# Optimization experiments

Measured on AMD Instinct MI355X. Metric: run time of the kernel, lower is better.

The kernel has to match this reference:

```python
import jax, jax.numpy as jnp
import numpy as np

NUM_HEADS = 8
DIM = 256
NW = 64  # number of windows per batch element


def setup_inputs() -> dict:
    key = jax.random.key(0)
    k_x, k_m, k_ws, k_wm, k_wp, k_bp = jax.random.split(key, 6)
    B_, N, C = 512, 128, DIM
    x = jax.random.normal(k_x, (B_, N, C), dtype=jnp.float32)
    # 0 / -100 additive attention mask (stand-in for the 0/-inf shift-window mask)
    mask = jnp.where(jax.random.uniform(k_m, (NW, N, N)) < 0.5, 0.0, -100.0).astype(jnp.float32)
    std = 0.02
    w_qkv_self = jax.random.normal(k_ws, (3 * C, C), dtype=jnp.float32) * std
    w_qkv_mut = jax.random.normal(k_wm, (3 * C, C), dtype=jnp.float32) * std
    w_proj = jax.random.normal(k_wp, (C, 2 * C), dtype=jnp.float32) * std
    b_proj = jax.random.normal(k_bp, (C,), dtype=jnp.float32) * std
    return {"x": x, "mask": mask, "w_qkv_self": w_qkv_self,
            "w_qkv_mut": w_qkv_mut, "w_proj": w_proj, "b_proj": b_proj}


def _split_qkv(x, w):
    # x: (B_, N, C); w: (3C, C) torch Linear weight -> y = x @ w.T
    B_, N, C = x.shape
    d = C // NUM_HEADS
    qkv = (x @ w.T).reshape(B_, N, 3, NUM_HEADS, d).transpose(2, 0, 3, 1, 4)
    return qkv[0], qkv[1], qkv[2]  # each (B_, H, N, d)


def _attention(q, k, v, mask, scale):
    # q,k,v: (B_, H, n, d); mask: (nW, Nfull, Nfull) additive
    B_, H, n, d = q.shape
    nW = mask.shape[0]
    attn = jnp.einsum('bhnd,bhmd->bhnm', q * scale, k)  # (B_, H, n, n)
    attn = attn.reshape(B_ // nW, nW, H, n, n) + mask[None, :, None, :n, :n]
    attn = jax.nn.softmax(attn.reshape(B_, H, n, n), axis=-1)
    out = jnp.einsum('bhnm,bhmd->bhnd', attn, v)
    return out.transpose(0, 2, 1, 3).reshape(B_, n, H * d)  # (B_, n, C)


def reference(x, mask, w_qkv_self, w_qkv_mut, w_proj, b_proj):
    B_, N, C = x.shape
    scale = (C // NUM_HEADS) ** (-0.5)
    # self window attention
    q, k, v = _split_qkv(x, w_qkv_self)
    x_out = _attention(q, k, v, mask, scale)  # (B_, N, C)
    # mutual (cross-frame) attention between the two halves of the window
    qm, km, vm = _split_qkv(x, w_qkv_mut)
    h = N // 2
    q1, q2 = qm[:, :, :h], qm[:, :, h:]
    k1, k2 = km[:, :, :h], km[:, :, h:]
    v1, v2 = vm[:, :, :h], vm[:, :, h:]
    x1_aligned = _attention(q2, k1, v1, mask, scale)  # (B_, N//2, C)
    x2_aligned = _attention(q1, k2, v2, mask, scale)  # (B_, N//2, C)
    x_mut = jnp.concatenate([x1_aligned, x2_aligned], axis=1)  # (B_, N, C)
    x_cat = jnp.concatenate([x_mut, x_out], axis=2)  # (B_, N, 2C)
    return x_cat @ w_proj.T + b_proj  # (B_, N, C)
```

## Files before the change

kernel.cpp:

```cpp
#include <hip/hip_runtime.h>
#include <stdint.h>

typedef __bf16 bf16x4 __attribute__((ext_vector_type(4)));
typedef __bf16 bf16x8 __attribute__((ext_vector_type(8)));
typedef float f32x4 __attribute__((ext_vector_type(4)));

#define DEVI __device__ __forceinline__

DEVI ushort bfbits(float f) {
  union { __bf16 b; ushort u; } v;
  v.b = (__bf16)f;
  return v.u;
}

DEVI void gload16(const void* g, void* l) {
  auto* gp = reinterpret_cast<const __attribute__((address_space(1))) uint32_t*>(
      reinterpret_cast<uintptr_t>(g));
  auto* lp = reinterpret_cast<__attribute__((address_space(3))) uint32_t*>(
      reinterpret_cast<uintptr_t>(l));
  __builtin_amdgcn_global_load_lds(gp, lp, 16, 0, 0);
}

__global__ __launch_bounds__(256) void cvt_x(const float* __restrict__ in,
                                             ushort* __restrict__ out) {
  int i = (blockIdx.x * 256 + threadIdx.x) * 4;
  float4 v = *(const float4*)(in + i);
  ushort4 o;
  o.x = bfbits(v.x); o.y = bfbits(v.y); o.z = bfbits(v.z); o.w = bfbits(v.w);
  *(ushort4*)(out + i) = o;
}

__global__ __launch_bounds__(256) void cvt_w(const float* __restrict__ ws,
                                             const float* __restrict__ wm,
                                             const float* __restrict__ wp,
                                             ushort* __restrict__ wqkv,
                                             ushort* __restrict__ wproj) {
  int i = blockIdx.x * 256 + threadIdx.x;
  if (i < 196608)       wqkv[i] = bfbits(ws[i]);
  else if (i < 393216)  wqkv[i] = bfbits(wm[i - 196608]);
  else                  wproj[i - 393216] = bfbits(wp[i - 393216]);
}

template <int KF, int NH>
DEVI void attn_body(const ushort* Qs, const ushort* Ks, const ushort* Vt,
                    ushort* Ps, const float* mrow, ushort* ob,
                    int qrow0, int kvbase, int orow0, int mrow0,
                    int lr, int lc) {
  f32x4 sacc[2][KF];
#pragma unroll
  for (int mf = 0; mf < 2; ++mf)
#pragma unroll
    for (int nf = 0; nf < KF; ++nf) sacc[mf][nf] = (f32x4){0.f, 0.f, 0.f, 0.f};

  bf16x8 aq[2];
#pragma unroll
  for (int mf = 0; mf < 2; ++mf) {
    int r = qrow0 + mf * 16 + lr;
    aq[mf] = *(const bf16x8*)(Qs + r * 32 + ((lc ^ ((r >> 1) & 3)) * 8));
  }
  __builtin_amdgcn_s_setprio(1);
#pragma unroll
  for (int nf = 0; nf < KF; ++nf) {
    int r = kvbase + nf * 16 + lr;
    bf16x8 bk = *(const bf16x8*)(Ks + r * 32 + ((lc ^ ((r >> 1) & 3)) * 8));
#pragma unroll
    for (int mf = 0; mf < 2; ++mf)
      sacc[mf][nf] = __builtin_amdgcn_mfma_f32_16x16x32_bf16(aq[mf], bk, sacc[mf][nf], 0, 0, 0);
  }
  __builtin_amdgcn_s_setprio(0);

#pragma unroll
  for (int mf = 0; mf < 2; ++mf)
#pragma unroll
    for (int nf = 0; nf < KF; ++nf)
#pragma unroll
      for (int r = 0; r < 4; ++r) {
        int row = mrow0 + mf * 16 + lc * 4 + r;
        int col = nf * 16 + lr;
        sacc[mf][nf][r] += mrow[row * 128 + col];
      }
#pragma unroll
  for (int mf = 0; mf < 2; ++mf)
#pragma unroll
    for (int r = 0; r < 4; ++r) {
      float mx = -1e30f;
#pragma unroll
      for (int nf = 0; nf < KF; ++nf) mx = fmaxf(mx, sacc[mf][nf][r]);
#pragma unroll
      for (int d = 1; d < 16; d <<= 1) mx = fmaxf(mx, __shfl_xor(mx, d));
      float s = 0.f;
#pragma unroll
      for (int nf = 0; nf < KF; ++nf) {
        float e = __expf(sacc[mf][nf][r] - mx);
        sacc[mf][nf][r] = e;
        s += e;
      }
#pragma unroll
      for (int d = 1; d < 16; d <<= 1) s += __shfl_xor(s, d);
      float inv = 1.f / s;
#pragma unroll
      for (int nf = 0; nf < KF; ++nf) sacc[mf][nf][r] *= inv;
    }

  f32x4 oacc[2][2];
#pragma unroll
  for (int mf = 0; mf < 2; ++mf)
#pragma unroll
    for (int nf = 0; nf < 2; ++nf) oacc[mf][nf] = (f32x4){0.f, 0.f, 0.f, 0.f};

#pragma unroll
  for (int hf = 0; hf < NH; ++hf) {
    __syncthreads();
#pragma unroll
    for (int mf = 0; mf < 2; ++mf)
#pragma unroll
      for (int r = 0; r < 4; ++r) {
        int prow = orow0 + mf * 16 + lc * 4 + r;
#pragma unroll
        for (int nf2 = 0; nf2 < 4; ++nf2) {
          int col = nf2 * 16 + lr;
          int grp = (col >> 3) ^ (prow & 7);
          Ps[prow * 64 + grp * 8 + (col & 7)] = bfbits(sacc[mf][hf * 4 + nf2][r]);
        }
      }
    __syncthreads();
    __builtin_amdgcn_s_setprio(1);
#pragma unroll
    for (int ks = 0; ks < 2; ++ks) {
      bf16x8 pf[2], vf[2];
#pragma unroll
      for (int mf = 0; mf < 2; ++mf) {
        int prow = orow0 + mf * 16 + lr;
        int grp = (ks * 4 + lc) ^ (prow & 7);
        pf[mf] = *(const bf16x8*)(Ps + prow * 64 + grp * 8);
      }
#pragma unroll
      for (int nf = 0; nf < 2; ++nf)
        vf[nf] = *(const bf16x8*)(Vt + (nf * 16 + lr) * 136 + kvbase + hf * 64 + ks * 32 + lc * 8);
#pragma unroll
      for (int mf = 0; mf < 2; ++mf)
#pragma unroll
        for (int nf = 0; nf < 2; ++nf)
          oacc[mf][nf] = __builtin_amdgcn_mfma_f32_16x16x32_bf16(pf[mf], vf[nf], oacc[mf][nf], 0, 0, 0);
    }
    __builtin_amdgcn_s_setprio(0);
  }

#pragma unroll
  for (int mf = 0; mf < 2; ++mf)
#pragma unroll
    for (int nf = 0; nf < 2; ++nf)
#pragma unroll
      for (int r = 0; r < 4; ++r) {
        int row = orow0 + mf * 16 + lc * 4 + r;
        int col = nf * 16 + lr;
        ob[(size_t)row * 512 + col] = bfbits(oacc[mf][nf][r]);
      }
}

__global__ __launch_bounds__(256) void attn_fused(const ushort* __restrict__ xb,
                                                  const ushort* __restrict__ wqkv,
                                                  const float* __restrict__ mask,
                                                  ushort* __restrict__ xcat) {
  __shared__ __align__(16) uint8_t smem[39424];
  ushort* Qs = (ushort*)smem;
  ushort* Vt = (ushort*)(smem + 8192);
  uint8_t* REGION = smem + 16896;
  ushort* Ks = (ushort*)REGION;
  ushort* xs = (ushort*)(REGION + 8192);
  ushort* wl = (ushort*)(REGION + 16384);
  ushort* Ps = (ushort*)REGION;

  const int bid = blockIdx.x;
  const int c = bid & 7;
  const int u = bid >> 3;
  const int m = u & 1;
  const int h = (u >> 1) & 7;
  const int b = (u >> 4) * 8 + c;
  const int wmask = b & 63;
  const int t = threadIdx.x;
  const int wid = t >> 6, l = t & 63;
  const int lr = l & 15, lc = l >> 4;
  const float scale = 0.17677669529663687f;

  const ushort* xrow = xb + (size_t)b * 128 * 256;
  const int wbase = m * 768;

  f32x4 pacc[2][6];
#pragma unroll
  for (int mf = 0; mf < 2; ++mf)
#pragma unroll
    for (int n = 0; n < 6; ++n) pacc[mf][n] = (f32x4){0.f, 0.f, 0.f, 0.f};

  for (int kk = 0; kk < 256; kk += 32) {
    __syncthreads();
#pragma unroll
    for (int p = 0; p < 2; ++p) {
      int slot = t + p * 256;
      int row = slot >> 2, cs = slot & 3;
      int cd = cs ^ ((row >> 1) & 3);
      gload16(xrow + (size_t)row * 256 + kk + cd * 8, xs + slot * 8);
    }
    {
      int slot = t;
      int row = slot >> 2, cs = slot & 3;
      int cd = cs ^ ((row >> 1) & 3);
      int grow = wbase + (row >> 5) * 256 + h * 32 + (row & 31);
      gload16(wqkv + (size_t)grow * 256 + kk + cd * 8, wl + slot * 8);
    }
    if (t < 128) {
      int slot = t + 256;
      int row = slot >> 2, cs = slot & 3;
      int cd = cs ^ ((row >> 1) & 3);
      int grow = wbase + (row >> 5) * 256 + h * 32 + (row & 31);
      gload16(wqkv + (size_t)grow * 256 + kk + cd * 8, wl + slot * 8);
    }
    __syncthreads();

    bf16x8 ax[2];
#pragma unroll
    for (int mf = 0; mf < 2; ++mf) {
      int r = wid * 32 + mf * 16 + lr;
      ax[mf] = *(const bf16x8*)(xs + r * 32 + ((lc ^ ((r >> 1) & 3)) * 8));
    }
    __builtin_amdgcn_s_setprio(1);
#pragma unroll
    for (int n = 0; n < 6; ++n) {
      int r = n * 16 + lr;
      bf16x8 bw = *(const bf16x8*)(wl + r * 32 + ((lc ^ ((r >> 1) & 3)) * 8));
#pragma unroll
      for (int mf = 0; mf < 2; ++mf)
        pacc[mf][n] = __builtin_amdgcn_mfma_f32_16x16x32_bf16(ax[mf], bw, pacc[mf][n], 0, 0, 0);
    }
    __builtin_amdgcn_s_setprio(0);
  }

#pragma unroll
  for (int mf = 0; mf < 2; ++mf) {
#pragma unroll
    for (int n = 0; n < 4; ++n)
#pragma unroll
      for (int j = 0; j < 4; ++j) {
        int row = wid * 32 + mf * 16 + lc * 4 + j;
        int d = (n & 1) * 16 + lr;
        float v = pacc[mf][n][j];
        if (n < 2) v *= scale;
        int sw = ((d >> 3) ^ ((row >> 1) & 3)) * 8 + (d & 7);
        (n < 2 ? Qs : Ks)[row * 32 + sw] = bfbits(v);
      }
#pragma unroll
    for (int k = 0; k < 2; ++k) {
      bf16x4 pk;
#pragma unroll
      for (int j = 0; j < 4; ++j) pk[j] = (__bf16)pacc[mf][4 + k][j];
      int d = k * 16 + lr;
      int row0 = wid * 32 + mf * 16 + lc * 4;
      *(bf16x4*)(Vt + d * 136 + row0) = pk;
    }
  }
  __syncthreads();

  const float* mrow = mask + (size_t)wmask * 128 * 128;

  if (m == 0) {
    ushort* ob = xcat + (size_t)b * 128 * 512 + 256 + h * 32;
    attn_body<8, 2>(Qs, Ks, Vt, Ps, mrow, ob,
                    wid * 32, 0,
                    wid * 32, wid * 32, lr, lc);
  } else {
    const int half = wid >> 1, sub = wid & 1;
    ushort* ob = xcat + (size_t)b * 128 * 512 + h * 32;
    attn_body<4, 1>(Qs, Ks, Vt, Ps, mrow, ob,
                    (half ? 0 : 64) + sub * 32, half ? 64 : 0,
                    half * 64 + sub * 32, sub * 32, lr, lc);
  }
}

__global__ __launch_bounds__(256) void gemm_proj(const ushort* __restrict__ A,
                                                 const ushort* __restrict__ B,
                                                 const float* __restrict__ bias,
                                                 float* __restrict__ out) {
  __shared__ ushort As[128 * 32];
  __shared__ ushort Bs[256 * 32];
  const int t = threadIdx.x, tm = blockIdx.x;
  const int w = t >> 6, l = t & 63;
  const int wr = (w >> 1) * 64, wc = (w & 1) * 128;
  const int lr = l & 15, lc = l >> 4;
  const ushort* Ab = A + (size_t)tm * 128 * 512;

  f32x4 acc[4][8];
#pragma unroll
  for (int m = 0; m < 4; ++m)
#pragma unroll
    for (int n = 0; n < 8; ++n) acc[m][n] = (f32x4){0.f, 0.f, 0.f, 0.f};

  for (int kk = 0; kk < 512; kk += 32) {
    __syncthreads();
#pragma unroll
    for (int p = 0; p < 2; ++p) {
      int slot = t + p * 256;
      int row = slot >> 2, cs = slot & 3;
      int cd = cs ^ ((row >> 1) & 3);
      gload16(Ab + (size_t)row * 512 + kk + cd * 8, As + slot * 8);
    }
#pragma unroll
    for (int p = 0; p < 4; ++p) {
      int slot = t + p * 256;
      int row = slot >> 2, cs = slot & 3;
      int cd = cs ^ ((row >> 1) & 3);
      gload16(B + (size_t)row * 512 + kk + cd * 8, Bs + slot * 8);
    }
    __syncthreads();

    bf16x8 af[4], bfr[8];
#pragma unroll
    for (int m = 0; m < 4; ++m) {
      int r = wr + m * 16 + lr;
      af[m] = *(const bf16x8*)(As + r * 32 + ((lc ^ ((r >> 1) & 3)) * 8));
    }
#pragma unroll
    for (int n = 0; n < 8; ++n) {
      int r = wc + n * 16 + lr;
      bfr[n] = *(const bf16x8*)(Bs + r * 32 + ((lc ^ ((r >> 1) & 3)) * 8));
    }
#pragma unroll
    for (int m = 0; m < 4; ++m)
#pragma unroll
      for (int n = 0; n < 8; ++n)
        acc[m][n] = __builtin_amdgcn_mfma_f32_16x16x32_bf16(af[m], bfr[n], acc[m][n], 0, 0, 0);
  }

#pragma unroll
  for (int m = 0; m < 4; ++m)
#pragma unroll
    for (int n = 0; n < 8; ++n)
#pragma unroll
      for (int r = 0; r < 4; ++r) {
        int row = tm * 128 + wr + m * 16 + lc * 4 + r;
        int col = wc + n * 16 + lr;
        out[(size_t)row * 256 + col] = acc[m][n][r] + bias[col];
      }
}

extern "C" void kernel_launch(void* const* d_in, const int* in_sizes, int n_in,
                              void* d_out, int out_size, void* d_ws, size_t ws_size,
                              hipStream_t stream) {
  const float* x = (const float*)d_in[0];
  const float* mask = (const float*)d_in[1];
  const float* w_qkv_self = (const float*)d_in[2];
  const float* w_qkv_mut = (const float*)d_in[3];
  const float* w_proj = (const float*)d_in[4];
  const float* b_proj = (const float*)d_in[5];
  float* out = (float*)d_out;

  uint8_t* ws = (uint8_t*)d_ws;
  ushort* xb    = (ushort*)(ws);
  ushort* wqkv  = (ushort*)(ws + 33554432);
  ushort* wproj = (ushort*)(ws + 34340864);
  ushort* xcat  = (ushort*)d_out;

  cvt_x<<<dim3(16384), dim3(256), 0, stream>>>(x, xb);
  cvt_w<<<dim3(2048), dim3(256), 0, stream>>>(w_qkv_self, w_qkv_mut, w_proj, wqkv, wproj);
  attn_fused<<<dim3(8192), dim3(256), 0, stream>>>(xb, wqkv, mask, xcat);
  gemm_proj<<<dim3(512), dim3(256), 0, stream>>>(xcat, wproj, b_proj, out);
}
```

Before: 204.2 us.

## Pre-transpose mask with log2e fold, use exp2, defer softmax normalization, prefetch QKV stage

Adds a kernel that transposes the mask per window and pre-multiplies it by log2(e), so attention can read four mask values per lane with one vector load instead of scalar strided loads. The Q scale also absorbs log2(e), which lets the softmax use the native exp2 and a reciprocal applied once to the output rather than to every probability. The QKV projection loop is restructured so the next K-slice is staged right after the MFMAs. Costs are one extra small launch and workspace buffer. The staging change only moves the load issue point, since one LDS buffer and a barrier remain between stages.

```diff
diff --git a/kernel.cpp b/kernel.cpp
--- a/kernel.cpp
+++ b/kernel.cpp
@@ -41,9 +41,33 @@
   else                  wproj[i - 393216] = bfbits(wp[i - 393216]);
 }
 
+__global__ __launch_bounds__(256) void cvt_mask(const float* __restrict__ mask,
+                                                float* __restrict__ maskT) {
+  __shared__ float tile[32][33];
+  const int w = blockIdx.x, tr = blockIdx.y, tc = blockIdx.z;
+  const float* src = mask + (size_t)w * 16384;
+  float* dst = maskT + (size_t)w * 16384;
+  const int t = threadIdx.x;
+  {
+    int r = t >> 3, c4 = (t & 7) * 4;
+    float4 v = *(const float4*)(src + (size_t)(tr * 32 + r) * 128 + tc * 32 + c4);
+    tile[r][c4 + 0] = v.x; tile[r][c4 + 1] = v.y;
+    tile[r][c4 + 2] = v.z; tile[r][c4 + 3] = v.w;
+  }
+  __syncthreads();
+  {
+    const float L2E = 1.4426950408889634f;
+    int c = t >> 3, r4 = (t & 7) * 4;
+    float4 o;
+    o.x = tile[r4 + 0][c] * L2E; o.y = tile[r4 + 1][c] * L2E;
+    o.z = tile[r4 + 2][c] * L2E; o.w = tile[r4 + 3][c] * L2E;
+    *(float4*)(dst + (size_t)(tc * 32 + c) * 128 + tr * 32 + r4) = o;
+  }
+}
+
 template <int KF, int NH>
 DEVI void attn_body(const ushort* Qs, const ushort* Ks, const ushort* Vt,
-                    ushort* Ps, const float* mrow, ushort* ob,
+                    ushort* Ps, const float* mT, ushort* ob,
                     int qrow0, int kvbase, int orow0, int mrow0,
                     int lr, int lc) {
   f32x4 sacc[2][KF];
@@ -72,13 +96,14 @@
 #pragma unroll
   for (int mf = 0; mf < 2; ++mf)
 #pragma unroll
-    for (int nf = 0; nf < KF; ++nf)
-#pragma unroll
-      for (int r = 0; r < 4; ++r) {
-        int row = mrow0 + mf * 16 + lc * 4 + r;
-        int col = nf * 16 + lr;
-        sacc[mf][nf][r] += mrow[row * 128 + col];
-      }
+    for (int nf = 0; nf < KF; ++nf) {
+      int col = nf * 16 + lr;
+      f32x4 mv = *(const f32x4*)(mT + (size_t)col * 128 + mrow0 + mf * 16 + lc * 4);
+#pragma unroll
+      for (int r = 0; r < 4; ++r) sacc[mf][nf][r] += mv[r];
+    }
+
+  float sinv[2][4];
 #pragma unroll
   for (int mf = 0; mf < 2; ++mf)
 #pragma unroll
@@ -91,15 +116,13 @@
       float s = 0.f;
 #pragma unroll
       for (int nf = 0; nf < KF; ++nf) {
-        float e = __expf(sacc[mf][nf][r] - mx);
+        float e = __builtin_amdgcn_exp2f(sacc[mf][nf][r] - mx);
         sacc[mf][nf][r] = e;
         s += e;
       }
 #pragma unroll
       for (int d = 1; d < 16; d <<= 1) s += __shfl_xor(s, d);
-      float inv = 1.f / s;
-#pragma unroll
-      for (int nf = 0; nf < KF; ++nf) sacc[mf][nf][r] *= inv;
+      sinv[mf][r] = __builtin_amdgcn_rcpf(s);
     }
 
   f32x4 oacc[2][2];
@@ -154,13 +177,13 @@
       for (int r = 0; r < 4; ++r) {
         int row = orow0 + mf * 16 + lc * 4 + r;
         int col = nf * 16 + lr;
-        ob[(size_t)row * 512 + col] = bfbits(oacc[mf][nf][r]);
+        ob[(size_t)row * 512 + col] = bfbits(oacc[mf][nf][r] * sinv[mf][r]);
       }
 }
 
 __global__ __launch_bounds__(256) void attn_fused(const ushort* __restrict__ xb,
                                                   const ushort* __restrict__ wqkv,
-                                                  const float* __restrict__ mask,
+                                                  const float* __restrict__ maskT,
                                                   ushort* __restrict__ xcat) {
   __shared__ __align__(16) uint8_t smem[39424];
   ushort* Qs = (ushort*)smem;
@@ -181,19 +204,12 @@
   const int t = threadIdx.x;
   const int wid = t >> 6, l = t & 63;
   const int lr = l & 15, lc = l >> 4;
-  const float scale = 0.17677669529663687f;
+  const float qscale = 0.17677669529663687f * 1.4426950408889634f;
 
   const ushort* xrow = xb + (size_t)b * 128 * 256;
   const int wbase = m * 768;
 
-  f32x4 pacc[2][6];
-#pragma unroll
-  for (int mf = 0; mf < 2; ++mf)
-#pragma unroll
-    for (int n = 0; n < 6; ++n) pacc[mf][n] = (f32x4){0.f, 0.f, 0.f, 0.f};
-
-  for (int kk = 0; kk < 256; kk += 32) {
-    __syncthreads();
+  auto STAGE = [&](int kk) {
 #pragma unroll
     for (int p = 0; p < 2; ++p) {
       int slot = t + p * 256;
@@ -215,6 +231,16 @@
       int grow = wbase + (row >> 5) * 256 + h * 32 + (row & 31);
       gload16(wqkv + (size_t)grow * 256 + kk + cd * 8, wl + slot * 8);
     }
+  };
+
+  f32x4 pacc[2][6];
+#pragma unroll
+  for (int mf = 0; mf < 2; ++mf)
+#pragma unroll
+    for (int n = 0; n < 6; ++n) pacc[mf][n] = (f32x4){0.f, 0.f, 0.f, 0.f};
+
+  STAGE(0);
+  for (int kk = 0; kk < 256; kk += 32) {
     __syncthreads();
 
     bf16x8 ax[2];
@@ -233,6 +259,11 @@
         pacc[mf][n] = __builtin_amdgcn_mfma_f32_16x16x32_bf16(ax[mf], bw, pacc[mf][n], 0, 0, 0);
     }
     __builtin_amdgcn_s_setprio(0);
+
+    if (kk < 224) {
+      __syncthreads();
+      STAGE(kk + 32);
+    }
   }
 
 #pragma unroll
@@ -244,7 +275,7 @@
         int row = wid * 32 + mf * 16 + lc * 4 + j;
         int d = (n & 1) * 16 + lr;
         float v = pacc[mf][n][j];
-        if (n < 2) v *= scale;
+        if (n < 2) v *= qscale;
         int sw = ((d >> 3) ^ ((row >> 1) & 3)) * 8 + (d & 7);
         (n < 2 ? Qs : Ks)[row * 32 + sw] = bfbits(v);
       }
@@ -260,17 +291,17 @@
   }
   __syncthreads();
 
-  const float* mrow = mask + (size_t)wmask * 128 * 128;
+  const float* mT = maskT + (size_t)wmask * 16384;
 
   if (m == 0) {
     ushort* ob = xcat + (size_t)b * 128 * 512 + 256 + h * 32;
-    attn_body<8, 2>(Qs, Ks, Vt, Ps, mrow, ob,
+    attn_body<8, 2>(Qs, Ks, Vt, Ps, mT, ob,
                     wid * 32, 0,
                     wid * 32, wid * 32, lr, lc);
   } else {
     const int half = wid >> 1, sub = wid & 1;
     ushort* ob = xcat + (size_t)b * 128 * 512 + h * 32;
-    attn_body<4, 1>(Qs, Ks, Vt, Ps, mrow, ob,
+    attn_body<4, 1>(Qs, Ks, Vt, Ps, mT, ob,
                     (half ? 0 : 64) + sub * 32, half ? 64 : 0,
                     half * 64 + sub * 32, sub * 32, lr, lc);
   }
@@ -357,10 +388,12 @@
   ushort* xb    = (ushort*)(ws);
   ushort* wqkv  = (ushort*)(ws + 33554432);
   ushort* wproj = (ushort*)(ws + 34340864);
+  float*  maskT = (float*)(ws + 34603008);
   ushort* xcat  = (ushort*)d_out;
 
   cvt_x<<<dim3(16384), dim3(256), 0, stream>>>(x, xb);
   cvt_w<<<dim3(2048), dim3(256), 0, stream>>>(w_qkv_self, w_qkv_mut, w_proj, wqkv, wproj);
-  attn_fused<<<dim3(8192), dim3(256), 0, stream>>>(xb, wqkv, mask, xcat);
+  cvt_mask<<<dim3(64, 4, 4), dim3(256), 0, stream>>>(mask, maskT);
+  attn_fused<<<dim3(8192), dim3(256), 0, stream>>>(xb, wqkv, maskT, xcat);
   gemm_proj<<<dim3(512), dim3(256), 0, stream>>>(xcat, wproj, b_proj, out);
 }
```

After: 261.1 us. +27.9%, slower.
